# Kernel optimization log

Measured on AMD Instinct MI355X. Metric: run time of the kernel, lower is better.

## Reference

```python
import jax, jax.numpy as jnp
import numpy as np

# Contact model constants (from ContactModel defaults / hardcoded values)
STIFFNESS = 100000.0
DISSIPATION = 0.2
STATIC_FRICTION = 0.8
DYNAMIC_FRICTION = 0.8
VISCOUS_FRICTION = 0.5
TRANSITION_VELOCITY = 0.2
GROUND_HEIGHT = 0.0
DT = 0.05
RADIUS = 0.032
EPS = 1e-5
EPS2 = 1e-16
BV = 50.0
BD = 300.0

# 12 spheres: 6 right (bodies 4,5), 6 left (bodies 9,10)
SPHERE_BODY = np.array([4, 4, 4, 4, 5, 5, 9, 9, 9, 9, 10, 10], dtype=np.int32)
SPHERE_LOCAL = np.array([
    [0.00190115788407966, -0.01, -0.00382630379623308],
    [0.148386399942063,   -0.01, -0.028713422052654],
    [0.133001170607051,   -0.01,  0.0516362473449566],
    [0.0662346661991635,  -0.01,  0.0263641606741698],
    [0.06,                -0.01, -0.0187603084619177],
    [0.045,               -0.01,  0.0618569567549652],
    [0.00190115788407966, -0.01,  0.00382630379623308],
    [0.148386399942063,   -0.01,  0.028713422052654],
    [0.133001170607051,   -0.01, -0.0516362473449566],
    [0.0662346661991635,  -0.01, -0.0263641606741698],
    [0.06,                -0.01,  0.0187603084619177],
    [0.045,               -0.01, -0.0618569567549652],
], dtype=np.float32)
NORMAL = np.array([0.0, 1.0, 0.0], dtype=np.float32)


def _sphere_positions(joints, joints_ori):
    # joints: (B,24,3), joints_ori: (B,24,3,3) -> (B,12,3)
    body_pos = joints[:, SPHERE_BODY]            # (B,12,3)
    body_ori = joints_ori[:, SPHERE_BODY]        # (B,12,3,3)
    local = jnp.asarray(SPHERE_LOCAL)
    return body_pos + jnp.einsum('bsij,sj->bsi', body_ori, local)


def _contact_forces(pos, vel):
    # pos, vel: (B,S,3) -> forces (B,S,3); fully vectorized over spheres
    n = jnp.asarray(NORMAL)
    indentation = GROUND_HEIGHT - pos[..., 1]                    # (B,S)
    vnormal = vel[..., 1]                                        # dot(vel, [0,1,0])
    vtangent = vel - vnormal[..., None] * n                      # (B,S,3)
    ind_vel = -vnormal
    k = 0.5 * STIFFNESS ** (2.0 / 3.0)
    # sqrt(ind^2+eps)**1.5 == (ind^2+eps)**0.75
    fH = (4.0 / 3.0) * k * np.sqrt(RADIUS * k) * (indentation * indentation + EPS) ** 0.75
    fHd = fH * (1.0 + 1.5 * DISSIPATION * ind_vel)
    fn = ((0.5 * jnp.tanh(BV * (ind_vel + 1.0 / (1.5 * DISSIPATION))) + 0.5 + EPS2)
          * (0.5 * jnp.tanh(BD * indentation) + 0.5 + EPS2) * fHd)
    vslip = jnp.sqrt(jnp.sum(vtangent * vtangent, axis=-1) + EPS)
    vrel = vslip / TRANSITION_VELOCITY
    ffriction = fn * (jnp.minimum(vrel, 1.0)
                      * (DYNAMIC_FRICTION + 2.0 * (STATIC_FRICTION - DYNAMIC_FRICTION) / (1.0 + vrel * vrel))
                      + VISCOUS_FRICTION * vslip)
    force = fn[..., None] * n
    friction_force = ffriction[..., None] * (-vtangent) / (vslip[..., None] + EPS)
    return force + friction_force


def _cop_and_torque(pos, forces):
    # pos, forces: (B,S,3) -> cop (B,3), torque (B,3); vectorized batch version of the per-b loop
    vf = forces[..., 1]                          # (B,S)
    valid = vf > 0.0
    w = jnp.where(valid, vf, 0.0)
    tw = jnp.sum(w, axis=-1)                     # (B,)
    has = tw > 0.0
    tw_safe = jnp.where(has, tw, 1.0)
    cop_x = jnp.where(has, jnp.sum(pos[..., 0] * w, axis=-1) / tw_safe, 0.0)
    cop_y = jnp.where(has, GROUND_HEIGHT, 0.0)
    cop_z = jnp.where(has, jnp.sum(pos[..., 2] * w, axis=-1) / tw_safe, 0.0)
    cop = jnp.stack([cop_x, cop_y, cop_z], axis=-1)  # (B,3)
    r = pos - cop[:, None, :]
    f_masked = jnp.where(valid[..., None], forces, 0.0)  # only valid contacts contribute torque
    torque = jnp.sum(jnp.cross(r, f_masked), axis=1)
    return cop, torque


def setup_inputs() -> dict:
    key = jax.random.key(0)
    k1, k2 = jax.random.split(key)
    B = 262144
    joints = jax.random.normal(k1, (B, 24, 3), dtype=jnp.float32)
    joints_ori = jax.random.normal(k2, (B, 24, 3, 3), dtype=jnp.float32)
    return {"joints": joints, "joints_ori": joints_ori}


def reference(joints, joints_ori):
    pos = _sphere_positions(joints, joints_ori)              # (B,12,3)
    # finite-difference sphere velocity over frames (dt); zero at first frame
    vel = (pos - jnp.concatenate([pos[:1], pos[:-1]], axis=0)) / DT
    sphere_forces = _contact_forces(pos, vel)                # (B,12,3)

    force = jnp.sum(sphere_forces, axis=1)
    force_right = jnp.sum(sphere_forces[:, :6], axis=1)
    force_left = jnp.sum(sphere_forces[:, 6:], axis=1)
    cop, torque = _cop_and_torque(pos, sphere_forces)
    cop_right, torque_right = _cop_and_torque(pos[:, :6], sphere_forces[:, :6])
    cop_left, torque_left = _cop_and_torque(pos[:, 6:], sphere_forces[:, 6:])
    return (force, torque, cop, sphere_forces, pos,
            force_right, force_left, torque_right, torque_left, cop_right, cop_left)
```

## Files before the change

### kernel.cpp

```cpp
#include <hip/hip_runtime.h>
#include <math.h>


__device__ __constant__ float c_local[12][3] = {
    {0.00190115788407966f, -0.01f, -0.00382630379623308f},
    {0.148386399942063f,   -0.01f, -0.028713422052654f},
    {0.133001170607051f,   -0.01f,  0.0516362473449566f},
    {0.0662346661991635f,  -0.01f,  0.0263641606741698f},
    {0.06f,                -0.01f, -0.0187603084619177f},
    {0.045f,               -0.01f,  0.0618569567549652f},
    {0.00190115788407966f, -0.01f,  0.00382630379623308f},
    {0.148386399942063f,   -0.01f,  0.028713422052654f},
    {0.133001170607051f,   -0.01f, -0.0516362473449566f},
    {0.0662346661991635f,  -0.01f, -0.0263641606741698f},
    {0.06f,                -0.01f,  0.0187603084619177f},
    {0.045f,               -0.01f, -0.0618569567549652f}};

__global__ __launch_bounds__(256)
void contact_kernel(const float* __restrict__ joints,
                    const float* __restrict__ jori,
                    float* __restrict__ out, const int B)
{
    const long t = (long)blockIdx.x * blockDim.x + threadIdx.x;
    if (t >= 2L * B) return;
    const int b = (int)(t >> 1);
    const int f = (int)(t & 1);

    float px[6], py[6], pz[6];
    float fx[6], fy[6], fz[6];

    {
        const int body0 = f ? 9 : 4;
        const int bodies[2] = {body0, body0 + 1};
        const int sbeg[2]   = {0, 4};
        const int scnt[2]   = {4, 2};
        const int bp = (b > 0) ? (b - 1) : b;
        const float* jr  = joints + (size_t)b  * 72;
        const float* jrp = joints + (size_t)bp * 72;
        const float* mr  = jori   + (size_t)b  * 216;
        const float* mrp = jori   + (size_t)bp * 216;

        #pragma unroll
        for (int bi = 0; bi < 2; ++bi) {
            const int body = bodies[bi];
            const float jx = jr[body*3+0], jy = jr[body*3+1], jz = jr[body*3+2];
            const float* m = mr + body*9;
            const float m00=m[0],m01=m[1],m02=m[2];
            const float m10=m[3],m11=m[4],m12=m[5];
            const float m20=m[6],m21=m[7],m22=m[8];
            const float kx = jrp[body*3+0], ky = jrp[body*3+1], kz = jrp[body*3+2];
            const float* nn = mrp + body*9;
            const float n00=nn[0],n01=nn[1],n02=nn[2];
            const float n10=nn[3],n11=nn[4],n12=nn[5];
            const float n20=nn[6],n21=nn[7],n22=nn[8];
            #pragma unroll
            for (int si = 0; si < 4; ++si) {
                if (si < scnt[bi]) {
                    const int s  = sbeg[bi] + si;
                    const int gs = f*6 + s;
                    const float lx = c_local[gs][0];
                    const float ly = c_local[gs][1];
                    const float lz = c_local[gs][2];
                    const float ax = jx + m00*lx + m01*ly + m02*lz;
                    const float ay = jy + m10*lx + m11*ly + m12*lz;
                    const float az = jz + m20*lx + m21*ly + m22*lz;
                    const float bx = kx + n00*lx + n01*ly + n02*lz;
                    const float by = ky + n10*lx + n11*ly + n12*lz;
                    const float bz = kz + n20*lx + n21*ly + n22*lz;
                    px[s] = ax; py[s] = ay; pz[s] = az;
                    fx[s] = (ax - bx) * 20.0f;
                    fy[s] = (ay - by) * 20.0f;
                    fz[s] = (az - bz) * 20.0f;
                }
            }
        }
    }

    const float KF  = 1077.21734501594f;
    const float CFH = (4.0f/3.0f) * KF * sqrtf(0.032f * KF);
    #pragma unroll
    for (int s = 0; s < 6; ++s) {
        const float vx = fx[s], vy = fy[s], vz = fz[s];
        const float ind     = -py[s];
        const float ind_vel = -vy;
        const float q   = ind*ind + 1e-5f;
        const float fH  = CFH * sqrtf(q * sqrtf(q));
        const float fHd = fH * (1.0f + 0.3f * ind_vel);
        const float t1 = (0.5f*tanhf(50.0f*(ind_vel + 3.3333333333333335f)) + 0.5f) + 1e-16f;
        const float t2 = (0.5f*tanhf(300.0f*ind) + 0.5f) + 1e-16f;
        const float fn = t1 * t2 * fHd;
        const float vslip = sqrtf(vx*vx + vz*vz + 1e-5f);
        const float vrel  = vslip * 5.0f;
        const float mu  = fminf(vrel, 1.0f) * 0.8f + 0.5f * vslip;
        const float ffr = fn * mu;
        const float sc  = ffr / (vslip + 1e-5f);
        fx[s] = -sc * vx;
        fy[s] = fn;
        fz[s] = -sc * vz;
    }

    float SFx=0.f,SFy=0.f,SFz=0.f;
    float SMx=0.f,SMy=0.f,SMz=0.f;
    float T0x=0.f,T0y=0.f,T0z=0.f;
    float tw=0.f, sx=0.f, sz=0.f;
    #pragma unroll
    for (int s = 0; s < 6; ++s) {
        SFx += fx[s]; SFy += fy[s]; SFz += fz[s];
        if (fy[s] > 0.f) {
            tw += fy[s]; sx += px[s]*fy[s]; sz += pz[s]*fy[s];
            SMx += fx[s]; SMy += fy[s]; SMz += fz[s];
            T0x += py[s]*fz[s] - pz[s]*fy[s];
            T0y += pz[s]*fx[s] - px[s]*fz[s];
            T0z += px[s]*fy[s] - py[s]*fx[s];
        }
    }

    const bool  hasf = tw > 0.f;
    const float cxf  = hasf ? sx / tw : 0.f;
    const float czf  = hasf ? sz / tw : 0.f;
    float Txf=0.f, Tyf=0.f, Tzf=0.f;
    #pragma unroll
    for (int s = 0; s < 6; ++s) {
        if (fy[s] > 0.f) {
            const float rx = px[s]-cxf, ry = py[s], rz = pz[s]-czf;
            Txf += ry*fz[s] - rz*fy[s];
            Tyf += rz*fx[s] - rx*fz[s];
            Tzf += rx*fy[s] - ry*fx[s];
        }
    }

    const float otw  = __shfl_xor(tw, 1),  osx  = __shfl_xor(sx, 1),  osz  = __shfl_xor(sz, 1);
    const float oFx  = __shfl_xor(SFx, 1), oFy  = __shfl_xor(SFy, 1), oFz  = __shfl_xor(SFz, 1);
    const float oMx  = __shfl_xor(SMx, 1), oMy  = __shfl_xor(SMy, 1), oMz  = __shfl_xor(SMz, 1);
    const float oT0x = __shfl_xor(T0x, 1), oT0y = __shfl_xor(T0y, 1), oT0z = __shfl_xor(T0z, 1);
    const float twa  = tw + otw;
    const bool  hasa = twa > 0.f;
    const float cxa  = hasa ? (sx + osx) / twa : 0.f;
    const float cza  = hasa ? (sz + osz) / twa : 0.f;
    const float aMx = SMx + oMx, aMy = SMy + oMy, aMz = SMz + oMz;
    const float Txa = (T0x + oT0x) + cza*aMy;
    const float Tya = (T0y + oT0y) - cza*aMx + cxa*aMz;
    const float Tza = (T0z + oT0z) - cxa*aMy;

    const size_t sB = (size_t)B;
    const size_t t3 = (size_t)b * 3;
    float* o;
    o = out + sB*(81 + f*3);  o[t3]=SFx; o[t3+1]=SFy; o[t3+2]=SFz;
    o = out + sB*(87 + f*3);  o[t3]=Txf; o[t3+1]=Tyf; o[t3+2]=Tzf;
    o = out + sB*(93 + f*3);  o[t3]=cxf; o[t3+1]=0.f; o[t3+2]=czf;
    if (f == 0) {
        o = out;          o[t3]=SFx+oFx; o[t3+1]=SFy+oFy; o[t3+2]=SFz+oFz;
        o = out + sB*3;   o[t3]=Txa;     o[t3+1]=Tya;     o[t3+2]=Tza;
        o = out + sB*6;   o[t3]=cxa;     o[t3+1]=0.f;     o[t3+2]=cza;
    }

    float* osf = out + sB*9  + (size_t)b*36 + f*18;
    float* opp = out + sB*45 + (size_t)b*36 + f*18;
    if ((B & 3) == 0) {
        float bufF[18], bufP[18];
        #pragma unroll
        for (int s = 0; s < 6; ++s) {
            bufF[s*3+0]=fx[s]; bufF[s*3+1]=fy[s]; bufF[s*3+2]=fz[s];
            bufP[s*3+0]=px[s]; bufP[s*3+1]=py[s]; bufP[s*3+2]=pz[s];
        }
        if (f == 0) {
            #pragma unroll
            for (int i = 0; i < 4; ++i) {
                reinterpret_cast<float4*>(osf)[i] = reinterpret_cast<const float4*>(bufF)[i];
                reinterpret_cast<float4*>(opp)[i] = reinterpret_cast<const float4*>(bufP)[i];
            }
            reinterpret_cast<float2*>(osf)[8] = make_float2(bufF[16], bufF[17]);
            reinterpret_cast<float2*>(opp)[8] = make_float2(bufP[16], bufP[17]);
        } else {
            reinterpret_cast<float2*>(osf)[0] = make_float2(bufF[0], bufF[1]);
            reinterpret_cast<float2*>(opp)[0] = make_float2(bufP[0], bufP[1]);
            #pragma unroll
            for (int i = 0; i < 4; ++i) {
                reinterpret_cast<float4*>(osf + 2)[i] =
                    make_float4(bufF[2+i*4], bufF[3+i*4], bufF[4+i*4], bufF[5+i*4]);
                reinterpret_cast<float4*>(opp + 2)[i] =
                    make_float4(bufP[2+i*4], bufP[3+i*4], bufP[4+i*4], bufP[5+i*4]);
            }
        }
    } else {
        #pragma unroll
        for (int s = 0; s < 6; ++s) {
            osf[s*3+0]=fx[s]; osf[s*3+1]=fy[s]; osf[s*3+2]=fz[s];
            opp[s*3+0]=px[s]; opp[s*3+1]=py[s]; opp[s*3+2]=pz[s];
        }
    }
}

extern "C" void kernel_launch(void* const* d_in, const int* in_sizes, int n_in,
                              void* d_out, int out_size, void* d_ws, size_t ws_size,
                              hipStream_t stream) {
    const float* joints = (const float*)d_in[0];
    const float* jori   = (const float*)d_in[1];
    float* out = (float*)d_out;
    const int B = in_sizes[0] / 72;
    const long threads = 2L * B;
    const int  block = 256;
    const int  grid  = (int)((threads + block - 1) / block);
    contact_kernel<<<grid, block, 0, stream>>>(joints, jori, out, B);
}
```

Measured before the change: 71.46 us.

## Process both feet per thread and drop cross-lane shuffle combine

```diff
diff --git a/kernel.cpp b/kernel.cpp
--- a/kernel.cpp
+++ b/kernel.cpp
@@ -16,179 +16,186 @@
     {0.06f,                -0.01f,  0.0187603084619177f},
     {0.045f,               -0.01f, -0.0618569567549652f}};
 
-__global__ __launch_bounds__(256)
+__global__ __launch_bounds__(256, 8)
 void contact_kernel(const float* __restrict__ joints,
                     const float* __restrict__ jori,
                     float* __restrict__ out, const int B)
 {
-    const long t = (long)blockIdx.x * blockDim.x + threadIdx.x;
-    if (t >= 2L * B) return;
-    const int b = (int)(t >> 1);
-    const int f = (int)(t & 1);
-
-    float px[6], py[6], pz[6];
-    float fx[6], fy[6], fz[6];
-
-    {
-        const int body0 = f ? 9 : 4;
-        const int bodies[2] = {body0, body0 + 1};
-        const int sbeg[2]   = {0, 4};
-        const int scnt[2]   = {4, 2};
-        const int bp = (b > 0) ? (b - 1) : b;
-        const float* jr  = joints + (size_t)b  * 72;
-        const float* jrp = joints + (size_t)bp * 72;
-        const float* mr  = jori   + (size_t)b  * 216;
-        const float* mrp = jori   + (size_t)bp * 216;
-
-        #pragma unroll
-        for (int bi = 0; bi < 2; ++bi) {
-            const int body = bodies[bi];
-            const float jx = jr[body*3+0], jy = jr[body*3+1], jz = jr[body*3+2];
-            const float* m = mr + body*9;
-            const float m00=m[0],m01=m[1],m02=m[2];
-            const float m10=m[3],m11=m[4],m12=m[5];
-            const float m20=m[6],m21=m[7],m22=m[8];
-            const float kx = jrp[body*3+0], ky = jrp[body*3+1], kz = jrp[body*3+2];
-            const float* nn = mrp + body*9;
-            const float n00=nn[0],n01=nn[1],n02=nn[2];
-            const float n10=nn[3],n11=nn[4],n12=nn[5];
-            const float n20=nn[6],n21=nn[7],n22=nn[8];
-            #pragma unroll
-            for (int si = 0; si < 4; ++si) {
-                if (si < scnt[bi]) {
-                    const int s  = sbeg[bi] + si;
-                    const int gs = f*6 + s;
-                    const float lx = c_local[gs][0];
-                    const float ly = c_local[gs][1];
-                    const float lz = c_local[gs][2];
-                    const float ax = jx + m00*lx + m01*ly + m02*lz;
-                    const float ay = jy + m10*lx + m11*ly + m12*lz;
-                    const float az = jz + m20*lx + m21*ly + m22*lz;
-                    const float bx = kx + n00*lx + n01*ly + n02*lz;
-                    const float by = ky + n10*lx + n11*ly + n12*lz;
-                    const float bz = kz + n20*lx + n21*ly + n22*lz;
-                    px[s] = ax; py[s] = ay; pz[s] = az;
-                    fx[s] = (ax - bx) * 20.0f;
-                    fy[s] = (ay - by) * 20.0f;
-                    fz[s] = (az - bz) * 20.0f;
-                }
-            }
-        }
-    }
+    const int b = blockIdx.x * blockDim.x + threadIdx.x;
+    if (b >= B) return;
+
+    const int bp = (b > 0) ? (b - 1) : b;
+    const float* jr  = joints + (size_t)b  * 72;
+    const float* jrp = joints + (size_t)bp * 72;
+    const float* mr  = jori   + (size_t)b  * 216;
+    const float* mrp = jori   + (size_t)bp * 216;
+    const size_t sB = (size_t)B;
+    const size_t t3 = (size_t)b * 3;
+
+    float aFx=0.f,aFy=0.f,aFz=0.f;
+    float aMx=0.f,aMy=0.f,aMz=0.f;
+    float aTx=0.f,aTy=0.f,aTz=0.f;
+    float atw=0.f,asx=0.f,asz=0.f;
 
     const float KF  = 1077.21734501594f;
     const float CFH = (4.0f/3.0f) * KF * sqrtf(0.032f * KF);
+
     #pragma unroll
-    for (int s = 0; s < 6; ++s) {
-        const float vx = fx[s], vy = fy[s], vz = fz[s];
-        const float ind     = -py[s];
-        const float ind_vel = -vy;
-        const float q   = ind*ind + 1e-5f;
-        const float fH  = CFH * sqrtf(q * sqrtf(q));
-        const float fHd = fH * (1.0f + 0.3f * ind_vel);
-        const float t1 = (0.5f*tanhf(50.0f*(ind_vel + 3.3333333333333335f)) + 0.5f) + 1e-16f;
-        const float t2 = (0.5f*tanhf(300.0f*ind) + 0.5f) + 1e-16f;
-        const float fn = t1 * t2 * fHd;
-        const float vslip = sqrtf(vx*vx + vz*vz + 1e-5f);
-        const float vrel  = vslip * 5.0f;
-        const float mu  = fminf(vrel, 1.0f) * 0.8f + 0.5f * vslip;
-        const float ffr = fn * mu;
-        const float sc  = ffr / (vslip + 1e-5f);
-        fx[s] = -sc * vx;
-        fy[s] = fn;
-        fz[s] = -sc * vz;
-    }
-
-    float SFx=0.f,SFy=0.f,SFz=0.f;
-    float SMx=0.f,SMy=0.f,SMz=0.f;
-    float T0x=0.f,T0y=0.f,T0z=0.f;
-    float tw=0.f, sx=0.f, sz=0.f;
-    #pragma unroll
-    for (int s = 0; s < 6; ++s) {
-        SFx += fx[s]; SFy += fy[s]; SFz += fz[s];
-        if (fy[s] > 0.f) {
-            tw += fy[s]; sx += px[s]*fy[s]; sz += pz[s]*fy[s];
-            SMx += fx[s]; SMy += fy[s]; SMz += fz[s];
-            T0x += py[s]*fz[s] - pz[s]*fy[s];
-            T0y += pz[s]*fx[s] - px[s]*fz[s];
-            T0z += px[s]*fy[s] - py[s]*fx[s];
-        }
-    }
-
-    const bool  hasf = tw > 0.f;
-    const float cxf  = hasf ? sx / tw : 0.f;
-    const float czf  = hasf ? sz / tw : 0.f;
-    float Txf=0.f, Tyf=0.f, Tzf=0.f;
-    #pragma unroll
-    for (int s = 0; s < 6; ++s) {
-        if (fy[s] > 0.f) {
-            const float rx = px[s]-cxf, ry = py[s], rz = pz[s]-czf;
-            Txf += ry*fz[s] - rz*fy[s];
-            Tyf += rz*fx[s] - rx*fz[s];
-            Tzf += rx*fy[s] - ry*fx[s];
-        }
-    }
-
-    const float otw  = __shfl_xor(tw, 1),  osx  = __shfl_xor(sx, 1),  osz  = __shfl_xor(sz, 1);
-    const float oFx  = __shfl_xor(SFx, 1), oFy  = __shfl_xor(SFy, 1), oFz  = __shfl_xor(SFz, 1);
-    const float oMx  = __shfl_xor(SMx, 1), oMy  = __shfl_xor(SMy, 1), oMz  = __shfl_xor(SMz, 1);
-    const float oT0x = __shfl_xor(T0x, 1), oT0y = __shfl_xor(T0y, 1), oT0z = __shfl_xor(T0z, 1);
-    const float twa  = tw + otw;
-    const bool  hasa = twa > 0.f;
-    const float cxa  = hasa ? (sx + osx) / twa : 0.f;
-    const float cza  = hasa ? (sz + osz) / twa : 0.f;
-    const float aMx = SMx + oMx, aMy = SMy + oMy, aMz = SMz + oMz;
-    const float Txa = (T0x + oT0x) + cza*aMy;
-    const float Tya = (T0y + oT0y) - cza*aMx + cxa*aMz;
-    const float Tza = (T0z + oT0z) - cxa*aMy;
-
-    const size_t sB = (size_t)B;
-    const size_t t3 = (size_t)b * 3;
-    float* o;
-    o = out + sB*(81 + f*3);  o[t3]=SFx; o[t3+1]=SFy; o[t3+2]=SFz;
-    o = out + sB*(87 + f*3);  o[t3]=Txf; o[t3+1]=Tyf; o[t3+2]=Tzf;
-    o = out + sB*(93 + f*3);  o[t3]=cxf; o[t3+1]=0.f; o[t3+2]=czf;
-    if (f == 0) {
-        o = out;          o[t3]=SFx+oFx; o[t3+1]=SFy+oFy; o[t3+2]=SFz+oFz;
-        o = out + sB*3;   o[t3]=Txa;     o[t3+1]=Tya;     o[t3+2]=Tza;
-        o = out + sB*6;   o[t3]=cxa;     o[t3+1]=0.f;     o[t3+2]=cza;
-    }
-
-    float* osf = out + sB*9  + (size_t)b*36 + f*18;
-    float* opp = out + sB*45 + (size_t)b*36 + f*18;
-    if ((B & 3) == 0) {
-        float bufF[18], bufP[18];
+    for (int f = 0; f < 2; ++f) {
+        float px[6], py[6], pz[6];
+        float fx[6], fy[6], fz[6];
+
+        {
+            const int body0 = (f == 0) ? 4 : 9;
+            const int sbeg[2] = {0, 4};
+            const int scnt[2] = {4, 2};
+            #pragma unroll
+            for (int bi = 0; bi < 2; ++bi) {
+                const int body = body0 + bi;
+                const float jx = jr[body*3+0], jy = jr[body*3+1], jz = jr[body*3+2];
+                const float* m = mr + body*9;
+                const float m00=m[0],m01=m[1],m02=m[2];
+                const float m10=m[3],m11=m[4],m12=m[5];
+                const float m20=m[6],m21=m[7],m22=m[8];
+                const float kx = jrp[body*3+0], ky = jrp[body*3+1], kz = jrp[body*3+2];
+                const float* nn = mrp + body*9;
+                const float n00=nn[0],n01=nn[1],n02=nn[2];
+                const float n10=nn[3],n11=nn[4],n12=nn[5];
+                const float n20=nn[6],n21=nn[7],n22=nn[8];
+                #pragma unroll
+                for (int si = 0; si < 4; ++si) {
+                    if (si < scnt[bi]) {
+                        const int s  = sbeg[bi] + si;
+                        const int gs = f*6 + s;
+                        const float lx = c_local[gs][0];
+                        const float ly = c_local[gs][1];
+                        const float lz = c_local[gs][2];
+                        const float ax = jx + m00*lx + m01*ly + m02*lz;
+                        const float ay = jy + m10*lx + m11*ly + m12*lz;
+                        const float az = jz + m20*lx + m21*ly + m22*lz;
+                        const float bx = kx + n00*lx + n01*ly + n02*lz;
+                        const float by = ky + n10*lx + n11*ly + n12*lz;
+                        const float bz = kz + n20*lx + n21*ly + n22*lz;
+                        px[s] = ax; py[s] = ay; pz[s] = az;
+                        fx[s] = (ax - bx) * 20.0f;
+                        fy[s] = (ay - by) * 20.0f;
+                        fz[s] = (az - bz) * 20.0f;
+                    }
+                }
+            }
+        }
+
         #pragma unroll
         for (int s = 0; s < 6; ++s) {
-            bufF[s*3+0]=fx[s]; bufF[s*3+1]=fy[s]; bufF[s*3+2]=fz[s];
-            bufP[s*3+0]=px[s]; bufP[s*3+1]=py[s]; bufP[s*3+2]=pz[s];
-        }
-        if (f == 0) {
-            #pragma unroll
-            for (int i = 0; i < 4; ++i) {
-                reinterpret_cast<float4*>(osf)[i] = reinterpret_cast<const float4*>(bufF)[i];
-                reinterpret_cast<float4*>(opp)[i] = reinterpret_cast<const float4*>(bufP)[i];
-            }
-            reinterpret_cast<float2*>(osf)[8] = make_float2(bufF[16], bufF[17]);
-            reinterpret_cast<float2*>(opp)[8] = make_float2(bufP[16], bufP[17]);
-        } else {
-            reinterpret_cast<float2*>(osf)[0] = make_float2(bufF[0], bufF[1]);
-            reinterpret_cast<float2*>(opp)[0] = make_float2(bufP[0], bufP[1]);
-            #pragma unroll
-            for (int i = 0; i < 4; ++i) {
-                reinterpret_cast<float4*>(osf + 2)[i] =
-                    make_float4(bufF[2+i*4], bufF[3+i*4], bufF[4+i*4], bufF[5+i*4]);
-                reinterpret_cast<float4*>(opp + 2)[i] =
-                    make_float4(bufP[2+i*4], bufP[3+i*4], bufP[4+i*4], bufP[5+i*4]);
-            }
-        }
-    } else {
+            const float vx = fx[s], vy = fy[s], vz = fz[s];
+            const float ind     = -py[s];
+            const float ind_vel = -vy;
+            const float q   = ind*ind + 1e-5f;
+            const float fH  = CFH * sqrtf(q * sqrtf(q));
+            const float fHd = fH * (1.0f + 0.3f * ind_vel);
+            const float t1 = (0.5f*tanhf(50.0f*(ind_vel + 3.3333333333333335f)) + 0.5f) + 1e-16f;
+            const float t2 = (0.5f*tanhf(300.0f*ind) + 0.5f) + 1e-16f;
+            const float fn = t1 * t2 * fHd;
+            const float vslip = sqrtf(vx*vx + vz*vz + 1e-5f);
+            const float vrel  = vslip * 5.0f;
+            const float mu  = fminf(vrel, 1.0f) * 0.8f + 0.5f * vslip;
+            const float ffr = fn * mu;
+            const float sc  = ffr / (vslip + 1e-5f);
+            fx[s] = -sc * vx;
+            fy[s] = fn;
+            fz[s] = -sc * vz;
+        }
+
+        float SFx=0.f,SFy=0.f,SFz=0.f;
+        float SMx=0.f,SMy=0.f,SMz=0.f;
+        float T0x=0.f,T0y=0.f,T0z=0.f;
+        float tw=0.f, sx=0.f, sz=0.f;
         #pragma unroll
         for (int s = 0; s < 6; ++s) {
-            osf[s*3+0]=fx[s]; osf[s*3+1]=fy[s]; osf[s*3+2]=fz[s];
-            opp[s*3+0]=px[s]; opp[s*3+1]=py[s]; opp[s*3+2]=pz[s];
-        }
+            SFx += fx[s]; SFy += fy[s]; SFz += fz[s];
+            if (fy[s] > 0.f) {
+                tw += fy[s]; sx += px[s]*fy[s]; sz += pz[s]*fy[s];
+                SMx += fx[s]; SMy += fy[s]; SMz += fz[s];
+                T0x += py[s]*fz[s] - pz[s]*fy[s];
+                T0y += pz[s]*fx[s] - px[s]*fz[s];
+                T0z += px[s]*fy[s] - py[s]*fx[s];
+            }
+        }
+
+        const bool  hasf = tw > 0.f;
+        const float cxf  = hasf ? sx / tw : 0.f;
+        const float czf  = hasf ? sz / tw : 0.f;
+        float Txf=0.f, Tyf=0.f, Tzf=0.f;
+        #pragma unroll
+        for (int s = 0; s < 6; ++s) {
+            if (fy[s] > 0.f) {
+                const float rx = px[s]-cxf, ry = py[s], rz = pz[s]-czf;
+                Txf += ry*fz[s] - rz*fy[s];
+                Tyf += rz*fx[s] - rx*fz[s];
+                Tzf += rx*fy[s] - ry*fx[s];
+            }
+        }
+
+        float* o;
+        o = out + sB*(81 + f*3);  o[t3]=SFx; o[t3+1]=SFy; o[t3+2]=SFz;
+        o = out + sB*(87 + f*3);  o[t3]=Txf; o[t3+1]=Tyf; o[t3+2]=Tzf;
+        o = out + sB*(93 + f*3);  o[t3]=cxf; o[t3+1]=0.f; o[t3+2]=czf;
+
+        float* osf = out + sB*9  + (size_t)b*36 + f*18;
+        float* opp = out + sB*45 + (size_t)b*36 + f*18;
+        if ((B & 3) == 0) {
+            float bufF[18], bufP[18];
+            #pragma unroll
+            for (int s = 0; s < 6; ++s) {
+                bufF[s*3+0]=fx[s]; bufF[s*3+1]=fy[s]; bufF[s*3+2]=fz[s];
+                bufP[s*3+0]=px[s]; bufP[s*3+1]=py[s]; bufP[s*3+2]=pz[s];
+            }
+            if (f == 0) {
+                #pragma unroll
+                for (int i = 0; i < 4; ++i) {
+                    reinterpret_cast<float4*>(osf)[i] =
+                        make_float4(bufF[i*4], bufF[i*4+1], bufF[i*4+2], bufF[i*4+3]);
+                    reinterpret_cast<float4*>(opp)[i] =
+                        make_float4(bufP[i*4], bufP[i*4+1], bufP[i*4+2], bufP[i*4+3]);
+                }
+                reinterpret_cast<float2*>(osf)[8] = make_float2(bufF[16], bufF[17]);
+                reinterpret_cast<float2*>(opp)[8] = make_float2(bufP[16], bufP[17]);
+            } else {
+                reinterpret_cast<float2*>(osf)[0] = make_float2(bufF[0], bufF[1]);
+                reinterpret_cast<float2*>(opp)[0] = make_float2(bufP[0], bufP[1]);
+                #pragma unroll
+                for (int i = 0; i < 4; ++i) {
+                    reinterpret_cast<float4*>(osf + 2)[i] =
+                        make_float4(bufF[2+i*4], bufF[3+i*4], bufF[4+i*4], bufF[5+i*4]);
+                    reinterpret_cast<float4*>(opp + 2)[i] =
+                        make_float4(bufP[2+i*4], bufP[3+i*4], bufP[4+i*4], bufP[5+i*4]);
+                }
+            }
+        } else {
+            #pragma unroll
+            for (int s = 0; s < 6; ++s) {
+                osf[s*3+0]=fx[s]; osf[s*3+1]=fy[s]; osf[s*3+2]=fz[s];
+                opp[s*3+0]=px[s]; opp[s*3+1]=py[s]; opp[s*3+2]=pz[s];
+            }
+        }
+
+        aFx += SFx; aFy += SFy; aFz += SFz;
+        aMx += SMx; aMy += SMy; aMz += SMz;
+        aTx += T0x; aTy += T0y; aTz += T0z;
+        atw += tw;  asx += sx;  asz += sz;
     }
+
+    const bool  hasa = atw > 0.f;
+    const float cxa  = hasa ? asx / atw : 0.f;
+    const float cza  = hasa ? asz / atw : 0.f;
+    const float Txa = aTx + cza*aMy;
+    const float Tya = aTy - cza*aMx + cxa*aMz;
+    const float Tza = aTz - cxa*aMy;
+
+    float* o;
+    o = out;          o[t3]=aFx; o[t3+1]=aFy; o[t3+2]=aFz;
+    o = out + sB*3;   o[t3]=Txa; o[t3+1]=Tya; o[t3+2]=Tza;
+    o = out + sB*6;   o[t3]=cxa; o[t3+1]=0.f; o[t3+2]=cza;
 }
 
 extern "C" void kernel_launch(void* const* d_in, const int* in_sizes, int n_in,
@@ -198,8 +205,7 @@
     const float* jori   = (const float*)d_in[1];
     float* out = (float*)d_out;
     const int B = in_sizes[0] / 72;
-    const long threads = 2L * B;
-    const int  block = 256;
-    const int  grid  = (int)((threads + block - 1) / block);
+    const int block = 256;
+    const int grid  = (B + block - 1) / block;
     contact_kernel<<<grid, block, 0, stream>>>(joints, jori, out, B);
 }
```

New measurement: 166.4 us. 2.33x slower.
